# Performance work log

Hardware: AMD Instinct MI355X
Metric: run time of the kernel (lower is better)

## Reference

```python
import jax, jax.numpy as jnp
import numpy as np

N = 50000
E = 800000
IN_CH = 2048
HID = 64      # hidden per head
HEADS = 4
OUT = 128
NEG_SLOPE = 0.2  # PyG GATv2Conv default
BN_EPS = 1e-5


def setup_inputs() -> dict:
    key = jax.random.key(0)
    ks = jax.random.split(key, 16)
    s = 0.02
    return {
        "x": jax.random.normal(ks[0], (N, IN_CH), jnp.float32),
        "edge_index": jax.random.randint(ks[1], (2, E), 0, N, jnp.int64),
        # conv1: in 2048 -> 4 heads x 64 (concat)
        "W1l": jax.random.normal(ks[2], (IN_CH, HEADS * HID), jnp.float32) * s,
        "W1r": jax.random.normal(ks[3], (IN_CH, HEADS * HID), jnp.float32) * s,
        "att1": jax.random.normal(ks[4], (HEADS, HID), jnp.float32) * s,
        "b1": jnp.zeros((HEADS * HID,), jnp.float32),
        # conv2: in 256 -> 1 head x 128 (no concat)
        "W2l": jax.random.normal(ks[5], (HEADS * HID, OUT), jnp.float32) * s,
        "W2r": jax.random.normal(ks[6], (HEADS * HID, OUT), jnp.float32) * s,
        "att2": jax.random.normal(ks[7], (1, OUT), jnp.float32) * s,
        "b2": jnp.zeros((OUT,), jnp.float32),
        # projection head: Linear -> BatchNorm1d -> ReLU -> Linear
        "pw1": jax.random.normal(ks[8], (OUT, OUT), jnp.float32) * s,
        "pb1": jnp.zeros((OUT,), jnp.float32),
        "gamma": jnp.ones((OUT,), jnp.float32),
        "beta": jnp.zeros((OUT,), jnp.float32),
        "pw2": jax.random.normal(ks[9], (OUT, OUT), jnp.float32) * s,
        "pb2": jnp.zeros((OUT,), jnp.float32),
    }


def gatv2_layer(x, src, dst, Wl, Wr, att, bias, heads, out_ch, concat):
    n = x.shape[0]
    xl = (x @ Wl).reshape(n, heads, out_ch)  # source-side transform
    xr = (x @ Wr).reshape(n, heads, out_ch)  # target-side transform
    # GATv2 score: a^T LeakyReLU(Wl x_j + Wr x_i) per edge, per head
    m = xl[src] + xr[dst]                              # [Et, H, C]
    e = jnp.einsum('ehc,hc->eh', jax.nn.leaky_relu(m, NEG_SLOPE), att)  # [Et, H]
    # segment softmax over incoming edges of each dst node
    emax = jax.ops.segment_max(e, dst, num_segments=n)  # [N, H]
    a = jnp.exp(e - emax[dst])
    denom = jax.ops.segment_sum(a, dst, num_segments=n)
    alpha = a / denom[dst]                              # [Et, H]
    out = jax.ops.segment_sum(alpha[:, :, None] * xl[src], dst, num_segments=n)  # [N, H, C]
    out = out.reshape(n, heads * out_ch) if concat else out.mean(axis=1)
    return out + bias


def reference(x, edge_index, W1l, W1r, att1, b1, W2l, W2r, att2, b2,
              pw1, pb1, gamma, beta, pw2, pb2):
    n = x.shape[0]
    loop = jnp.arange(n, dtype=edge_index.dtype)
    src = jnp.concatenate([edge_index[0], loop])  # add self loops (PyG default)
    dst = jnp.concatenate([edge_index[1], loop])

    h = gatv2_layer(x, src, dst, W1l, W1r, att1, b1, HEADS, HID, concat=True)
    h = jax.nn.relu(h)
    h = gatv2_layer(h, src, dst, W2l, W2r, att2, b2, 1, OUT, concat=False)

    # projection head (BatchNorm1d with batch statistics, training-mode math)
    h = h @ pw1 + pb1
    mu = h.mean(axis=0)
    var = h.var(axis=0)
    h = (h - mu) * jax.lax.rsqrt(var + BN_EPS) * gamma + beta
    h = jax.nn.relu(h)
    return h @ pw2 + pb2
```

## Files before the change

kernel.cpp:

```cpp
#include <hip/hip_runtime.h>
#include <hip/hip_bf16.h>
#include <cstdint>
#include <cstddef>

#define NN 50000
#define NE 800000
#define ETOT (NN + NE)

typedef float f32x4 __attribute__((ext_vector_type(4)));
typedef short s16x8 __attribute__((ext_vector_type(8)));

__device__ __forceinline__ unsigned short f2bf(float f) {
  unsigned u = __float_as_uint(f);
  u += 0x7FFFu + ((u >> 16) & 1u);
  return (unsigned short)(u >> 16);
}
__device__ __forceinline__ float bf2f(unsigned short u) {
  return __uint_as_float(((unsigned)u) << 16);
}
__device__ __forceinline__ unsigned cvtpk(float lo, float hi) {
  unsigned r;
  asm("v_cvt_pk_bf16_f32 %0, %1, %2" : "=v"(r) : "v"(lo), "v"(hi));
  return r;
}
typedef const __attribute__((address_space(1))) void* gas_t;
typedef __attribute__((address_space(3))) void* las_t;
__device__ __forceinline__ void gload_lds16(const void* g, void* l) {
  __builtin_amdgcn_global_load_lds((gas_t)g, (las_t)l, 16, 0, 0);
}

__global__ void detect_i64(const void* __restrict__ ei, int* __restrict__ flag) {
  const long long v = ((const long long*)ei)[threadIdx.x];
  const bool ok = (v >= 0 && v < NN);
  const unsigned long long m = __ballot(ok);
  if (threadIdx.x == 0) *flag = (m == ~0ULL) ? 1 : 0;
}
__device__ __forceinline__ void load_edge(const void* __restrict__ ei, int is64,
                                          int eidx, int& src, int& dst) {
  if (eidx >= NE) { src = dst = eidx - NE; return; }
  if (is64) {
    src = (int)((const long long*)ei)[eidx];
    dst = (int)((const long long*)ei)[NE + eidx];
  } else {
    src = ((const int*)ei)[eidx];
    dst = ((const int*)ei)[NE + eidx];
  }
}

__global__ __launch_bounds__(256) void csr_hist(
    const void* __restrict__ ei, const int* __restrict__ flag, int* __restrict__ cnt)
{
  const int e = blockIdx.x * 256 + threadIdx.x;
  if (e >= ETOT) return;
  int src, dst;
  load_edge(ei, *flag, e, src, dst);
  atomicAdd(&cnt[dst], 1);
}

__global__ __launch_bounds__(256) void scan_blk(
    const int* __restrict__ cnt, int* __restrict__ rp1, int* __restrict__ bsum)
{
  const int tid = threadIdx.x, lane = tid & 63, w = tid >> 6;
  const int i = blockIdx.x * 256 + tid;
  int s = (i < NN) ? cnt[i] : 0;
  #pragma unroll
  for (int off = 1; off < 64; off <<= 1) {
    int t = __shfl_up(s, off);
    if (lane >= off) s += t;
  }
  __shared__ int wsum[4];
  if (lane == 63) wsum[w] = s;
  __syncthreads();
  int add = 0;
  #pragma unroll
  for (int k = 0; k < 4; ++k) if (k < w) add += wsum[k];
  s += add;
  if (i < NN) rp1[i] = s;
  if (tid == 255) bsum[blockIdx.x] = s;
}

__global__ __launch_bounds__(256) void scan_tops(int* __restrict__ bsum, int nb)
{
  const int tid = threadIdx.x, lane = tid & 63, w = tid >> 6;
  int s = (tid < nb) ? bsum[tid] : 0;
  #pragma unroll
  for (int off = 1; off < 64; off <<= 1) {
    int t = __shfl_up(s, off);
    if (lane >= off) s += t;
  }
  __shared__ int wsum[4];
  if (lane == 63) wsum[w] = s;
  __syncthreads();
  int add = 0;
  #pragma unroll
  for (int k = 0; k < 4; ++k) if (k < w) add += wsum[k];
  s += add;
  if (tid < nb) bsum[tid] = s;
}

__global__ __launch_bounds__(256) void scan_add(
    const int* __restrict__ bsum, int* __restrict__ rowptr)
{
  const int i = blockIdx.x * 256 + threadIdx.x;
  if (i == 0) rowptr[0] = 0;
  if (i < NN) rowptr[i + 1] += (blockIdx.x > 0) ? bsum[blockIdx.x - 1] : 0;
}

__global__ __launch_bounds__(256) void csr_scatter(
    const void* __restrict__ ei, const int* __restrict__ flag,
    const int* __restrict__ rowptr, int* __restrict__ cur, int* __restrict__ colv)
{
  const int e = blockIdx.x * 256 + threadIdx.x;
  if (e >= ETOT) return;
  int src, dst;
  load_edge(ei, *flag, e, src, dst);
  const int pos = atomicAdd(&cur[dst], 1);
  colv[rowptr[dst] + pos] = src;
}

template<int AMODE>
__global__ __launch_bounds__(256) void gemm_t(
    const void* __restrict__ Av, const unsigned short* __restrict__ BT,
    void* __restrict__ Cv, const float* __restrict__ bias,
    const float* __restrict__ abn,
    int M, int K, int Ncols, int out_bf16, int nbx, int nwg)
{
  constexpr bool AF32 = (AMODE > 0);
  __shared__ __align__(16) unsigned char Araw[2][AF32 ? 128 * 32 * 4 : 128 * 32 * 2];
  __shared__ __align__(16) unsigned short Bs[2][128 * 32];

  int bid = blockIdx.x;
  {
    const int q = nwg >> 3, r = nwg & 7;
    const int xcd = bid & 7, idx = bid >> 3;
    bid = (xcd < r ? xcd * (q + 1) : r * (q + 1) + (xcd - r) * q) + idx;
  }
  const int bx = bid % nbx, by = bid / nbx;
  const int row0 = by * 128, col0 = bx * 128;
  const int tid = threadIdx.x, wave = tid >> 6, lane = tid & 63;
  const int l16 = lane & 15, lq = lane >> 4;
  const int wr = wave >> 1, wc = wave & 1;

  const unsigned short* Abf = (const unsigned short*)Av;
  const float*          Af  = (const float*)Av;

  f32x4 acc[4][4];
  #pragma unroll
  for (int i = 0; i < 4; ++i)
    #pragma unroll
    for (int j = 0; j < 4; ++j)
      #pragma unroll
      for (int r = 0; r < 4; ++r) acc[i][j][r] = 0.f;

  auto stageA = [&](int buf, int k0) {
    if constexpr (AF32) {
      #pragma unroll
      for (int j = 0; j < 4; ++j) {
        const int c = tid + 256 * j;
        const int row = c >> 3;
        const int kg = (c & 7) ^ (row & 7);
        int gr = row0 + row; if (gr >= M) gr = M - 1;
        gload_lds16(Af + (size_t)gr * K + k0 + kg * 4, Araw[buf] + c * 16);
      }
    } else {
      #pragma unroll
      for (int j = 0; j < 2; ++j) {
        const int c = tid + 256 * j;
        const int row = c >> 2, part = c & 3;
        int gr = row0 + row; if (gr >= M) gr = M - 1;
        gload_lds16(Abf + (size_t)gr * K + k0 + part * 8, Araw[buf] + c * 16);
      }
    }
  };
  auto stageB = [&](int buf, int k0) {
    #pragma unroll
    for (int j = 0; j < 2; ++j) {
      const int c = tid + 256 * j;
      const int row = c >> 2, part = c & 3;
      gload_lds16(BT + (size_t)(col0 + row) * K + k0 + part * 8,
                  (unsigned char*)Bs[buf] + c * 16);
    }
  };

  const int nt = K >> 5;
  stageA(0, 0);
  stageB(0, 0);
  __syncthreads();

  for (int t = 0; t < nt; ++t) {
    const int cur = t & 1, nxt = cur ^ 1;
    if (t + 1 < nt) {
      stageA(nxt, (t + 1) << 5);
      stageB(nxt, (t + 1) << 5);
    }

    s16x8 af[4], bf[4];
    if constexpr (AF32) {
      const float* Ab = (const float*)Araw[cur];
      float sc[8], sh[8];
      if constexpr (AMODE == 2) {
        const int kb = (t << 5) + lq * 8;
        *(float4*)&sc[0] = *(const float4*)(abn + kb);
        *(float4*)&sc[4] = *(const float4*)(abn + kb + 4);
        *(float4*)&sh[0] = *(const float4*)(abn + K + kb);
        *(float4*)&sh[4] = *(const float4*)(abn + K + kb + 4);
      }
      #pragma unroll
      for (int f = 0; f < 4; ++f) {
        const int row = wr * 64 + f * 16 + l16;
        const int s0 = (row << 3) + ((2 * lq)     ^ (row & 7));
        const int s1 = (row << 3) + ((2 * lq + 1) ^ (row & 7));
        float4 f0 = *(const float4*)(Ab + s0 * 4);
        float4 f1 = *(const float4*)(Ab + s1 * 4);
        if constexpr (AMODE == 2) {
          f0.x = fmaxf(f0.x * sc[0] + sh[0], 0.f);
          f0.y = fmaxf(f0.y * sc[1] + sh[1], 0.f);
          f0.z = fmaxf(f0.z * sc[2] + sh[2], 0.f);
          f0.w = fmaxf(f0.w * sc[3] + sh[3], 0.f);
          f1.x = fmaxf(f1.x * sc[4] + sh[4], 0.f);
          f1.y = fmaxf(f1.y * sc[5] + sh[5], 0.f);
          f1.z = fmaxf(f1.z * sc[6] + sh[6], 0.f);
          f1.w = fmaxf(f1.w * sc[7] + sh[7], 0.f);
        }
        uint4 w;
        w.x = cvtpk(f0.x, f0.y); w.y = cvtpk(f0.z, f0.w);
        w.z = cvtpk(f1.x, f1.y); w.w = cvtpk(f1.z, f1.w);
        af[f] = *(s16x8*)&w;
      }
    } else {
      const unsigned short* Ab = (const unsigned short*)Araw[cur];
      #pragma unroll
      for (int f = 0; f < 4; ++f)
        af[f] = *(const s16x8*)&Ab[(wr * 64 + f * 16 + l16) * 32 + lq * 8];
    }
    #pragma unroll
    for (int f = 0; f < 4; ++f)
      bf[f] = *(const s16x8*)&Bs[cur][(wc * 64 + f * 16 + l16) * 32 + lq * 8];

    #pragma unroll
    for (int fm = 0; fm < 4; ++fm)
      #pragma unroll
      for (int fn = 0; fn < 4; ++fn)
        acc[fm][fn] = __builtin_amdgcn_mfma_f32_16x16x32_bf16(af[fm], bf[fn], acc[fm][fn], 0, 0, 0);

    __syncthreads();
  }

  float bv[4];
  #pragma unroll
  for (int fn = 0; fn < 4; ++fn)
    bv[fn] = bias ? bias[col0 + wc * 64 + fn * 16 + l16] : 0.f;

  #pragma unroll
  for (int fm = 0; fm < 4; ++fm) {
    #pragma unroll
    for (int r = 0; r < 4; ++r) {
      const int row = row0 + wr * 64 + fm * 16 + lq * 4 + r;
      if (row < M) {
        #pragma unroll
        for (int fn = 0; fn < 4; ++fn) {
          const int col = col0 + wc * 64 + fn * 16 + l16;
          const float v = acc[fm][fn][r] + bv[fn];
          if (out_bf16) ((unsigned short*)Cv)[(size_t)row * Ncols + col] = f2bf(v);
          else          ((float*)Cv)[(size_t)row * Ncols + col] = v;
        }
      }
    }
  }
}

__global__ __launch_bounds__(256) void node_conv1(
    const unsigned short* __restrict__ H1, const int* __restrict__ rowptr,
    const int* __restrict__ colv, const float* __restrict__ att,
    const float* __restrict__ b1, unsigned short* __restrict__ out)
{
  const int node = blockIdx.x * 4 + (threadIdx.x >> 6);
  if (node >= NN) return;
  const int lane = threadIdx.x & 63;
  const int base4 = lane * 4;
  float xr[4], at[4];
  {
    const ushort4 t = *(const ushort4*)&H1[(size_t)node * 512 + 256 + base4];
    xr[0] = bf2f(t.x); xr[1] = bf2f(t.y); xr[2] = bf2f(t.z); xr[3] = bf2f(t.w);
    at[0] = att[base4]; at[1] = att[base4 + 1]; at[2] = att[base4 + 2]; at[3] = att[base4 + 3];
  }
  float m = -1e30f, s = 0.f, a0 = 0.f, a1 = 0.f, a2 = 0.f, a3 = 0.f;
  const int beg = rowptr[node], end = rowptr[node + 1];
  ushort4 xa = *(const ushort4*)&H1[(size_t)colv[beg] * 512 + base4];
  ushort4 xb = (beg + 1 < end) ? *(const ushort4*)&H1[(size_t)colv[beg + 1] * 512 + base4] : xa;
  for (int i = beg; i < end; ++i) {
    const int ip2 = (i + 2 < end) ? i + 2 : end - 1;
    const ushort4 xc = *(const ushort4*)&H1[(size_t)colv[ip2] * 512 + base4];
    const float x0 = bf2f(xa.x), x1 = bf2f(xa.y), x2 = bf2f(xa.z), x3 = bf2f(xa.w);
    float mm, e = 0.f;
    mm = x0 + xr[0]; mm = mm > 0.f ? mm : 0.2f * mm; e += mm * at[0];
    mm = x1 + xr[1]; mm = mm > 0.f ? mm : 0.2f * mm; e += mm * at[1];
    mm = x2 + xr[2]; mm = mm > 0.f ? mm : 0.2f * mm; e += mm * at[2];
    mm = x3 + xr[3]; mm = mm > 0.f ? mm : 0.2f * mm; e += mm * at[3];
    e += __shfl_xor(e, 1); e += __shfl_xor(e, 2);
    e += __shfl_xor(e, 4); e += __shfl_xor(e, 8);
    const float mn = fmaxf(m, e);
    const float sc = __expf(m - mn);
    const float w  = __expf(e - mn);
    s = s * sc + w;
    a0 = a0 * sc + w * x0; a1 = a1 * sc + w * x1;
    a2 = a2 * sc + w * x2; a3 = a3 * sc + w * x3;
    m = mn;
    xa = xb; xb = xc;
  }
  const float inv = 1.f / s;
  ushort4 o;
  o.x = f2bf(fmaxf(a0 * inv + b1[base4],     0.f));
  o.y = f2bf(fmaxf(a1 * inv + b1[base4 + 1], 0.f));
  o.z = f2bf(fmaxf(a2 * inv + b1[base4 + 2], 0.f));
  o.w = f2bf(fmaxf(a3 * inv + b1[base4 + 3], 0.f));
  *(ushort4*)&out[(size_t)node * 256 + base4] = o;
}

__global__ __launch_bounds__(256) void node_conv2(
    const unsigned short* __restrict__ H2, const int* __restrict__ rowptr,
    const int* __restrict__ colv, const float* __restrict__ att,
    const float* __restrict__ b2, unsigned short* __restrict__ out)
{
  const int node = blockIdx.x * 4 + (threadIdx.x >> 6);
  if (node >= NN) return;
  const int lane = threadIdx.x & 63;
  const int c2 = lane * 2;
  float xr0, xr1, at0, at1;
  {
    const ushort2 t = *(const ushort2*)&H2[(size_t)node * 256 + 128 + c2];
    xr0 = bf2f(t.x); xr1 = bf2f(t.y);
    at0 = att[c2]; at1 = att[c2 + 1];
  }
  float m = -1e30f, s = 0.f, a0 = 0.f, a1 = 0.f;
  const int beg = rowptr[node], end = rowptr[node + 1];
  ushort2 xa = *(const ushort2*)&H2[(size_t)colv[beg] * 256 + c2];
  ushort2 xb = (beg + 1 < end) ? *(const ushort2*)&H2[(size_t)colv[beg + 1] * 256 + c2] : xa;
  for (int i = beg; i < end; ++i) {
    const int ip2 = (i + 2 < end) ? i + 2 : end - 1;
    const ushort2 xc = *(const ushort2*)&H2[(size_t)colv[ip2] * 256 + c2];
    const float x0 = bf2f(xa.x), x1 = bf2f(xa.y);
    float mm, e = 0.f;
    mm = x0 + xr0; mm = mm > 0.f ? mm : 0.2f * mm; e += mm * at0;
    mm = x1 + xr1; mm = mm > 0.f ? mm : 0.2f * mm; e += mm * at1;
    #pragma unroll
    for (int off = 32; off > 0; off >>= 1) e += __shfl_xor(e, off);
    const float mn = fmaxf(m, e);
    const float sc = __expf(m - mn);
    const float w  = __expf(e - mn);
    s = s * sc + w;
    a0 = a0 * sc + w * x0; a1 = a1 * sc + w * x1;
    m = mn;
    xa = xb; xb = xc;
  }
  const float inv = 1.f / s;
  ushort2 o;
  o.x = f2bf(a0 * inv + b2[c2]);
  o.y = f2bf(a1 * inv + b2[c2 + 1]);
  *(ushort2*)&out[(size_t)node * 128 + c2] = o;
}

__global__ __launch_bounds__(256) void wt_cvt(
    const float* __restrict__ Wa, const float* __restrict__ Wb,
    unsigned short* __restrict__ dst, int K, int halfN)
{
  const int k = blockIdx.x * 256 + threadIdx.x;
  const int n = blockIdx.y;
  if (k >= K) return;
  const float v = (n < halfN) ? Wa[(size_t)k * halfN + n]
                              : Wb[(size_t)k * halfN + (n - halfN)];
  dst[(size_t)n * K + k] = f2bf(v);
}

#define SROWS 256
__global__ __launch_bounds__(256) void bn_stats(
    const float* __restrict__ t, float* __restrict__ sums, int M)
{
  const int tid = threadIdx.x;
  const int c = tid & 127, half = tid >> 7;
  const int r0 = blockIdx.x * SROWS;
  int rend = r0 + SROWS; if (rend > M) rend = M;
  float s = 0.f, q = 0.f;
  for (int r = r0 + half; r < rend; r += 2) {
    const float v = t[(size_t)r * 128 + c];
    s += v; q += v * v;
  }
  __shared__ float ls[256], lq[256];
  ls[tid] = s; lq[tid] = q;
  __syncthreads();
  if (tid < 128) {
    atomicAdd(&sums[c],       ls[tid] + ls[tid + 128]);
    atomicAdd(&sums[128 + c], lq[tid] + lq[tid + 128]);
  }
}

__global__ void bn_final(const float* __restrict__ sums, const float* __restrict__ gamma,
                         const float* __restrict__ beta, float* __restrict__ bnp, int M)
{
  const int c = threadIdx.x;
  if (c < 128) {
    const float mu  = sums[c] / (float)M;
    const float var = sums[128 + c] / (float)M - mu * mu;
    const float sc  = gamma[c] * rsqrtf(var + 1e-5f);
    bnp[c] = sc;
    bnp[128 + c] = beta[c] - mu * sc;
  }
}

extern "C" void kernel_launch(void* const* d_in, const int* in_sizes, int n_in,
                              void* d_out, int out_size, void* d_ws, size_t ws_size,
                              hipStream_t stream)
{
  (void)in_sizes; (void)n_in; (void)out_size; (void)ws_size;
  const float* x     = (const float*)d_in[0];
  const void*  ei    = (const void*)d_in[1];
  const float* W1l   = (const float*)d_in[2];
  const float* W1r   = (const float*)d_in[3];
  const float* att1  = (const float*)d_in[4];
  const float* b1    = (const float*)d_in[5];
  const float* W2l   = (const float*)d_in[6];
  const float* W2r   = (const float*)d_in[7];
  const float* att2  = (const float*)d_in[8];
  const float* b2    = (const float*)d_in[9];
  const float* pw1   = (const float*)d_in[10];
  const float* pb1   = (const float*)d_in[11];
  const float* gamma = (const float*)d_in[12];
  const float* beta  = (const float*)d_in[13];
  const float* pw2   = (const float*)d_in[14];
  const float* pb2   = (const float*)d_in[15];

  char* ws = (char*)d_ws;
  unsigned short* H1b   = (unsigned short*)(ws + 0);
  unsigned short* h1b   = (unsigned short*)(ws + 51200000);
  unsigned short* H2b   = (unsigned short*)(ws + 76800000);
  unsigned short* h2b   = (unsigned short*)(ws + 102400000);
  float*          tbuf  = (float*)(ws + 115200000);
  int*            rowptr = (int*)(ws + 153600000);
  int*            cnt    = (int*)(ws + 153800192);
  int*            colv   = (int*)(ws + 154000384);
  unsigned short* WT1    = (unsigned short*)(ws + 157400384);
  unsigned short* WT2    = (unsigned short*)(ws + 159497536);
  unsigned short* PT1    = (unsigned short*)(ws + 159628608);
  unsigned short* PT2    = (unsigned short*)(ws + 159661376);
  float*          bnsum  = (float*)(ws + 159694144);
  float*          bnp    = (float*)(ws + 159695168);
  int*            eflag  = (int*)(ws + 159696192);
  int*            bsum   = (int*)(ws + 159696256);

  hipMemsetAsync(cnt, 0, 200000, stream);
  hipMemsetAsync(bnsum, 0, 1024, stream);

  detect_i64<<<1, 64, 0, stream>>>(ei, eflag);
  wt_cvt<<<dim3(8, 512), 256, 0, stream>>>(W1l, W1r, WT1, 2048, 256);
  wt_cvt<<<dim3(1, 256), 256, 0, stream>>>(W2l, W2r, WT2, 256, 128);
  wt_cvt<<<dim3(1, 128), 256, 0, stream>>>(pw1, pw1, PT1, 128, 128);
  wt_cvt<<<dim3(1, 128), 256, 0, stream>>>(pw2, pw2, PT2, 128, 128);

  const int ebl = (ETOT + 255) / 256;
  const int nsb = (NN + 255) / 256;
  csr_hist<<<ebl, 256, 0, stream>>>(ei, eflag, cnt);
  scan_blk<<<nsb, 256, 0, stream>>>(cnt, rowptr + 1, bsum);
  scan_tops<<<1, 256, 0, stream>>>(bsum, nsb);
  scan_add<<<nsb, 256, 0, stream>>>(bsum, rowptr);
  hipMemsetAsync(cnt, 0, 200000, stream);
  csr_scatter<<<ebl, 256, 0, stream>>>(ei, eflag, rowptr, cnt, colv);

  const int nby = (NN + 127) / 128;
  gemm_t<1><<<nby * 4, 256, 0, stream>>>(x, WT1, H1b, nullptr, nullptr, NN, 2048, 512, 1, 4, nby * 4);
  node_conv1<<<(NN + 3) / 4, 256, 0, stream>>>(H1b, rowptr, colv, att1, b1, h1b);

  gemm_t<0><<<nby * 2, 256, 0, stream>>>(h1b, WT2, H2b, nullptr, nullptr, NN, 256, 256, 1, 2, nby * 2);
  node_conv2<<<(NN + 3) / 4, 256, 0, stream>>>(H2b, rowptr, colv, att2, b2, h2b);

  gemm_t<0><<<nby, 256, 0, stream>>>(h2b, PT1, tbuf, pb1, nullptr, NN, 128, 128, 0, 1, nby);
  bn_stats<<<(NN + SROWS - 1) / SROWS, 256, 0, stream>>>(tbuf, bnsum, NN);
  bn_final<<<1, 128, 0, stream>>>(bnsum, gamma, beta, bnp, NN);
  gemm_t<2><<<nby, 256, 0, stream>>>(tbuf, PT2, (float*)d_out, pb2, bnp, NN, 128, 128, 0, 1, nby);
}
```

Measured before the change: 643.7 us.

## Triple-buffer GEMM LDS staging with explicit vmcnt waits and tiled weight transpose

```diff
diff --git a/kernel.cpp b/kernel.cpp
--- a/kernel.cpp
+++ b/kernel.cpp
@@ -126,8 +126,9 @@
     int M, int K, int Ncols, int out_bf16, int nbx, int nwg)
 {
   constexpr bool AF32 = (AMODE > 0);
-  __shared__ __align__(16) unsigned char Araw[2][AF32 ? 128 * 32 * 4 : 128 * 32 * 2];
-  __shared__ __align__(16) unsigned short Bs[2][128 * 32];
+  constexpr int ABYTES = AF32 ? 128 * 32 * 4 : 128 * 32 * 2;
+  __shared__ __align__(16) unsigned char Araw[3][ABYTES];
+  __shared__ __align__(16) unsigned short Bs[3][128 * 32];
 
   int bid = blockIdx.x;
   {
@@ -183,16 +184,18 @@
   };
 
   const int nt = K >> 5;
-  stageA(0, 0);
-  stageB(0, 0);
-  __syncthreads();
-
+  stageA(0, 0);  stageB(0, 0);
+  stageA(1, 32); stageB(1, 32);
+  if constexpr (AF32) asm volatile("s_waitcnt vmcnt(6)" ::: "memory");
+  else                asm volatile("s_waitcnt vmcnt(4)" ::: "memory");
+  __builtin_amdgcn_sched_barrier(0);
+  __builtin_amdgcn_s_barrier();
+  __builtin_amdgcn_sched_barrier(0);
+
+  int cur = 0;
   for (int t = 0; t < nt; ++t) {
-    const int cur = t & 1, nxt = cur ^ 1;
-    if (t + 1 < nt) {
-      stageA(nxt, (t + 1) << 5);
-      stageB(nxt, (t + 1) << 5);
-    }
+    int pf = cur - 1; if (pf < 0) pf += 3;
+    if (t + 2 < nt) { stageA(pf, (t + 2) << 5); stageB(pf, (t + 2) << 5); }
 
     s16x8 af[4], bf[4];
     if constexpr (AF32) {
@@ -237,13 +240,26 @@
     for (int f = 0; f < 4; ++f)
       bf[f] = *(const s16x8*)&Bs[cur][(wc * 64 + f * 16 + l16) * 32 + lq * 8];
 
+    __builtin_amdgcn_s_setprio(1);
     #pragma unroll
     for (int fm = 0; fm < 4; ++fm)
       #pragma unroll
       for (int fn = 0; fn < 4; ++fn)
         acc[fm][fn] = __builtin_amdgcn_mfma_f32_16x16x32_bf16(af[fm], bf[fn], acc[fm][fn], 0, 0, 0);
-
-    __syncthreads();
+    __builtin_amdgcn_s_setprio(0);
+
+    if (t + 1 < nt) {
+      if (t + 2 < nt) {
+        if constexpr (AF32) asm volatile("s_waitcnt vmcnt(6)" ::: "memory");
+        else                asm volatile("s_waitcnt vmcnt(4)" ::: "memory");
+      } else {
+        asm volatile("s_waitcnt vmcnt(0)" ::: "memory");
+      }
+      __builtin_amdgcn_sched_barrier(0);
+      __builtin_amdgcn_s_barrier();
+      __builtin_amdgcn_sched_barrier(0);
+    }
+    cur = (cur == 2) ? 0 : cur + 1;
   }
 
   float bv[4];
@@ -360,16 +376,26 @@
   *(ushort2*)&out[(size_t)node * 128 + c2] = o;
 }
 
-__global__ __launch_bounds__(256) void wt_cvt(
+__global__ __launch_bounds__(256) void wt_cvt_t(
     const float* __restrict__ Wa, const float* __restrict__ Wb,
     unsigned short* __restrict__ dst, int K, int halfN)
 {
-  const int k = blockIdx.x * 256 + threadIdx.x;
-  const int n = blockIdx.y;
-  if (k >= K) return;
-  const float v = (n < halfN) ? Wa[(size_t)k * halfN + n]
-                              : Wb[(size_t)k * halfN + (n - halfN)];
-  dst[(size_t)n * K + k] = f2bf(v);
+  __shared__ float tile[64][65];
+  const int k0 = blockIdx.x * 64, n0 = blockIdx.y * 64;
+  const int tx = threadIdx.x & 63, ty = threadIdx.x >> 6;
+  const float* W = (n0 < halfN) ? Wa : Wb;
+  const int nb = (n0 < halfN) ? n0 : n0 - halfN;
+  #pragma unroll
+  for (int j = 0; j < 16; ++j) {
+    const int kl = ty * 16 + j;
+    tile[kl][tx] = W[(size_t)(k0 + kl) * halfN + nb + tx];
+  }
+  __syncthreads();
+  #pragma unroll
+  for (int j = 0; j < 16; ++j) {
+    const int nl = ty * 16 + j;
+    dst[(size_t)(n0 + nl) * K + k0 + tx] = f2bf(tile[tx][nl]);
+  }
 }
 
 #define SROWS 256
@@ -451,10 +477,10 @@
   hipMemsetAsync(bnsum, 0, 1024, stream);
 
   detect_i64<<<1, 64, 0, stream>>>(ei, eflag);
-  wt_cvt<<<dim3(8, 512), 256, 0, stream>>>(W1l, W1r, WT1, 2048, 256);
-  wt_cvt<<<dim3(1, 256), 256, 0, stream>>>(W2l, W2r, WT2, 256, 128);
-  wt_cvt<<<dim3(1, 128), 256, 0, stream>>>(pw1, pw1, PT1, 128, 128);
-  wt_cvt<<<dim3(1, 128), 256, 0, stream>>>(pw2, pw2, PT2, 128, 128);
+  wt_cvt_t<<<dim3(32, 8), 256, 0, stream>>>(W1l, W1r, WT1, 2048, 256);
+  wt_cvt_t<<<dim3(4, 4), 256, 0, stream>>>(W2l, W2r, WT2, 256, 128);
+  wt_cvt_t<<<dim3(2, 2), 256, 0, stream>>>(pw1, pw1, PT1, 128, 128);
+  wt_cvt_t<<<dim3(2, 2), 256, 0, stream>>>(pw2, pw2, PT2, 128, 128);
 
   const int ebl = (ETOT + 255) / 256;
   const int nsb = (NN + 255) / 256;
```

Result: slower. 717.9 us (+11.5%).
